# Kernel tuning notes

Hardware: AMD Instinct MI355X
Metric: run time of the kernel (lower is better)

## Reference

```python
import jax, jax.numpy as jnp
import numpy as np

DIM = 768
NUM_HEADS = 12
HEAD_DIM = DIM // NUM_HEADS
SCALE = HEAD_DIM ** -0.5


def setup_inputs() -> dict:
    key = jax.random.key(0)
    k_x, k_qkv, k_pw, k_pb = jax.random.split(key, 4)
    x = jax.random.normal(k_x, (1, 4096, DIM), dtype=jnp.float32)
    # nn.Linear weights stored as [out, in]; apply as x @ W.T
    w_qkv = jax.random.normal(k_qkv, (3 * DIM, DIM), dtype=jnp.float32) * (DIM ** -0.5)
    w_proj = jax.random.normal(k_pw, (DIM, DIM), dtype=jnp.float32) * (DIM ** -0.5)
    b_proj = jax.random.normal(k_pb, (DIM,), dtype=jnp.float32) * 0.01
    return {"x": x, "w_qkv": w_qkv, "w_proj": w_proj, "b_proj": b_proj}


def reference(x, w_qkv, w_proj, b_proj):
    b, s, d = x.shape
    qkv = jnp.einsum('bsd,ed->bse', x, w_qkv)            # [B,S,3D]
    qkv = qkv.reshape(b, s, 3, NUM_HEADS, HEAD_DIM)
    qkv = jnp.transpose(qkv, (2, 0, 3, 1, 4))            # [3,B,H,S,hd]
    q, k, v = qkv[0], qkv[1], qkv[2]
    scores = jnp.einsum('bhqe,bhke->bhqk', q, k) * SCALE  # [B,H,S,S]
    probs = jax.nn.softmax(scores, axis=-1)
    attended = jnp.einsum('bhqk,bhke->bhqe', probs, v)    # [B,H,S,hd]
    attended = jnp.transpose(attended, (0, 2, 1, 3)).reshape(b, s, d)
    return jnp.einsum('bsd,ed->bse', attended, w_proj) + b_proj
```

## Files before the change

### kernel.cpp

```cpp
#include <hip/hip_runtime.h>
#include <hip/hip_bf16.h>

using short8 = __attribute__((ext_vector_type(8))) short;
using s16x4  = __attribute__((ext_vector_type(4))) short;
using f32x2  = __attribute__((ext_vector_type(2))) float;
using f32x4  = __attribute__((ext_vector_type(4))) float;
using f32x16 = __attribute__((ext_vector_type(16))) float;
using v2i    = __attribute__((ext_vector_type(2))) int;

#define DIM   768
#define D3    2304
#define SEQL  4096
#define NHEAD 12
#define NSPLIT 3

#if defined(__has_builtin)
#  if __has_builtin(__builtin_amdgcn_permlane32_swap)
#    define HAVE_PLSWAP 1
#  endif
#endif

static __device__ __forceinline__ short f2bs(float f) {
  union { __hip_bfloat16 h; short s; } u;
  u.h = __float2bfloat16(f);
  return u.s;
}

static __device__ __forceinline__ float bf2f(short s) {
  union { unsigned u; float f; } x;
  x.u = ((unsigned)(unsigned short)s) << 16;
  return x.f;
}

static __device__ __forceinline__ int cvtpk(float lo, float hi) {
  int r;
  asm("v_cvt_pk_bf16_f32 %0, %1, %2" : "=v"(r) : "v"(lo), "v"(hi));
  return r;
}

static __device__ __forceinline__ f32x2 pkadd(f32x2 a, f32x2 b) {
  f32x2 r;
  asm("v_pk_add_f32 %0, %1, %2" : "=v"(r) : "v"(a), "v"(b));
  return r;
}

static __device__ __forceinline__ float ex2(float x) {
  float r;
  asm("v_exp_f32 %0, %1" : "=v"(r) : "v"(x));
  return r;
}

static __device__ __forceinline__ void gl_lds16(const void* g, void* lds) {
  __builtin_amdgcn_global_load_lds((const __attribute__((address_space(1))) void*)g,
                                   (__attribute__((address_space(3))) void*)lds, 16, 0, 0);
}

__global__ __launch_bounds__(256) void cvt3_kernel(const float* __restrict__ x,
                                                   const float* __restrict__ wq,
                                                   const float* __restrict__ wp,
                                                   short* __restrict__ xb,
                                                   short* __restrict__ wqb,
                                                   short* __restrict__ wpb) {
  int b = blockIdx.x;
  const float* src; short* dst; int base; float sc = 1.0f;
  if (b < 3072)      { src = x;  dst = xb;  base = b * 1024; }
  else if (b < 4800) { src = wq; dst = wqb; base = (b - 3072) * 1024;
                       if (base < DIM * DIM) sc = 0.125f * 1.4426950408889634f; }
  else               { src = wp; dst = wpb; base = (b - 4800) * 1024; }
  int i = base + threadIdx.x * 4;
  f32x4 v = *(const f32x4*)(src + i);
  s16x4 o;
  #pragma unroll
  for (int j = 0; j < 4; ++j) o[j] = f2bs(v[j] * sc);
  *(s16x4*)(dst + i) = o;
}

template <bool BF16OUT>
__global__ __launch_bounds__(256) void gemm_bt(const short* __restrict__ A,
                                               const short* __restrict__ B,
                                               short* __restrict__ Cb,
                                               float* __restrict__ Cf,
                                               const float* __restrict__ bias,
                                               int M, int N, int K) {
  __shared__ short As[128 * 64];
  __shared__ short Bs[128 * 64];
  const int tid = threadIdx.x;
  const int l  = tid & 63;
  const int w  = tid >> 6;
  const int g  = l >> 4, lc = l & 15;
  const int wr = w >> 1, wc = w & 1;
  const int m0 = blockIdx.y * 128, n0 = blockIdx.x * 128;
  const int trow = tid >> 3;
  const int tcol = (tid & 7) * 8;

  f32x4 acc[4][4];
  #pragma unroll
  for (int a = 0; a < 4; ++a)
    #pragma unroll
    for (int b = 0; b < 4; ++b) acc[a][b] = (f32x4){0.f, 0.f, 0.f, 0.f};

  for (int k0 = 0; k0 < K; k0 += 64) {
    __syncthreads();
    #pragma unroll
    for (int i = 0; i < 4; ++i) {
      int row = i * 32 + trow;
      gl_lds16(A + (size_t)(m0 + row) * K + k0 + tcol, As + row * 64 + tcol);
      gl_lds16(B + (size_t)(n0 + row) * K + k0 + tcol, Bs + row * 64 + tcol);
    }
    __syncthreads();
    #pragma unroll
    for (int kk = 0; kk < 2; ++kk) {
      short8 af[4], bf[4];
      #pragma unroll
      for (int mt = 0; mt < 4; ++mt)
        af[mt] = *(const short8*)(As + (wr * 64 + mt * 16 + lc) * 64 + kk * 32 + g * 8);
      #pragma unroll
      for (int nt = 0; nt < 4; ++nt)
        bf[nt] = *(const short8*)(Bs + (wc * 64 + nt * 16 + lc) * 64 + kk * 32 + g * 8);
      #pragma unroll
      for (int mt = 0; mt < 4; ++mt)
        #pragma unroll
        for (int nt = 0; nt < 4; ++nt)
          acc[mt][nt] = __builtin_amdgcn_mfma_f32_16x16x32_bf16(af[mt], bf[nt], acc[mt][nt], 0, 0, 0);
    }
  }

  #pragma unroll
  for (int mt = 0; mt < 4; ++mt)
    #pragma unroll
    for (int nt = 0; nt < 4; ++nt)
      #pragma unroll
      for (int r = 0; r < 4; ++r) {
        int row = m0 + wr * 64 + mt * 16 + g * 4 + r;
        int col = n0 + wc * 64 + nt * 16 + lc;
        float v = acc[mt][nt][r];
        if (BF16OUT) Cb[(size_t)row * N + col] = f2bs(v);
        else         Cf[(size_t)row * N + col] = v + bias[col];
      }
}

__global__ __launch_bounds__(256) void transpose_v(const short* __restrict__ qkv,
                                                   short* __restrict__ vtg) {
  __shared__ short T[64][72];
  const int jt = blockIdx.x, hd = blockIdx.y, tid = threadIdx.x;
  #pragma unroll
  for (int i = 0; i < 2; ++i) {
    int idx = i * 256 + tid;
    int r = idx >> 3, c = idx & 7;
    *(short8*)&T[r][8 * c] =
        *(const short8*)(qkv + (size_t)(jt * 64 + r) * D3 + 1536 + hd * 64 + 8 * c);
  }
  __syncthreads();
  #pragma unroll
  for (int i = 0; i < 2; ++i) {
    int idx = i * 256 + tid;
    int d = idx >> 3, jc = idx & 7;
    short8 v;
    #pragma unroll
    for (int e = 0; e < 8; ++e) v[e] = T[8 * jc + e][d];
    *(short8*)(vtg + ((size_t)hd * 64 + d) * 4096 + jt * 64 + 8 * jc) = v;
  }
}

__global__ __launch_bounds__(512) void attn_kernel(const short* __restrict__ qkv,
                                                   const short* __restrict__ vtg,
                                                   short* __restrict__ O0,
                                                   short* __restrict__ O1,
                                                   short* __restrict__ O2,
                                                   float* __restrict__ Lp) {
  __shared__ short Ks[2][64 * 64];
  __shared__ short Vt[2][64 * 64];

  const int tid = threadIdx.x;
  const int l = tid & 63, w = tid >> 6;
  const int h = l >> 5;
  const int q5 = l & 31;
  const int head = blockIdx.y;
  const int hoff = head * 64;
  const int qbase = blockIdx.x * 256 + w * 32;
  const int z = blockIdx.z;
  const int t0 = (z * 64) / 3, tend = ((z + 1) * 64) / 3;

  short8 qf[4];
  {
    const short* qrow = qkv + (size_t)(qbase + q5) * D3 + hoff;
    #pragma unroll
    for (int ks = 0; ks < 4; ++ks) qf[ks] = *(const short8*)(qrow + ks * 16 + h * 8);
  }

  f32x16 o[2];
  #pragma unroll
  for (int nt = 0; nt < 2; ++nt)
    #pragma unroll
    for (int r = 0; r < 16; ++r) o[nt][r] = 0.f;
  float l_run = 0.f;
  const f32x16 zacc = {};

  const int swzK = 8 * (q5 & 7);

  const int srow = tid >> 3, scol = (tid & 7) * 8;
  const int sswz = 8 * (srow & 7);
  const short* kptr = qkv + (size_t)(t0 * 64 + srow) * D3 + hoff + 768 + (scol ^ sswz);
  const short* vptr = vtg + ((size_t)hoff + srow) * 4096 + t0 * 64 + (scol ^ sswz);

  #define STAGE_KV(BUF)                                                          \
    {                                                                            \
      gl_lds16(kptr, &Ks[BUF][tid * 8]);                                         \
      gl_lds16(vptr, &Vt[BUF][tid * 8]);                                         \
      kptr += 64 * D3;                                                           \
      vptr += 64;                                                                \
    }

  STAGE_KV(0);
  asm volatile("s_waitcnt vmcnt(0)" ::: "memory");
  __syncthreads();

  for (int tt = t0; tt < tend; ++tt) {
    const int cur = (tt - t0) & 1;
    const bool pre = (tt + 1 < tend);
    if (pre) STAGE_KV(cur ^ 1);

    f32x16 p[2];
    __builtin_amdgcn_s_setprio(1);
    #pragma unroll
    for (int ks = 0; ks < 4; ++ks) {
      #pragma unroll
      for (int mt = 0; mt < 2; ++mt) {
        short8 kf = *(const short8*)(&Ks[cur][(mt * 32 + q5) * 64
                                              + ((ks * 16 + h * 8) ^ swzK)]);
        p[mt] = __builtin_amdgcn_mfma_f32_32x32x16_bf16(kf, qf[ks],
                                                        ks == 0 ? zacc : p[mt], 0, 0, 0);
      }
    }
    __builtin_amdgcn_s_setprio(0);

    f32x2 s2 = {0.f, 0.f};
    #pragma unroll
    for (int mt = 0; mt < 2; ++mt)
      #pragma unroll
      for (int i = 0; i < 8; ++i) {
        float pe0 = ex2(p[mt][2 * i]);
        float pe1 = ex2(p[mt][2 * i + 1]);
        p[mt][2 * i] = pe0;
        p[mt][2 * i + 1] = pe1;
        s2 = pkadd(s2, (f32x2){pe0, pe1});
      }
    l_run += s2[0] + s2[1];

    int D[16];
    #pragma unroll
    for (int mt = 0; mt < 2; ++mt)
      #pragma unroll
      for (int c = 0; c < 4; ++c) {
        D[mt * 8 + c * 2 + 0] = cvtpk(p[mt][4 * c + 0], p[mt][4 * c + 1]);
        D[mt * 8 + c * 2 + 1] = cvtpk(p[mt][4 * c + 2], p[mt][4 * c + 3]);
      }

    __builtin_amdgcn_s_setprio(1);
    #pragma unroll
    for (int ks = 0; ks < 4; ++ks) {
      union { int i[4]; short8 s; } pa;
#ifdef HAVE_PLSWAP
      v2i r02 = __builtin_amdgcn_permlane32_swap(D[4 * ks + 0], D[4 * ks + 2], false, false);
      v2i r13 = __builtin_amdgcn_permlane32_swap(D[4 * ks + 1], D[4 * ks + 3], false, false);
      pa.i[0] = r02[0];
      pa.i[1] = r13[0];
      pa.i[2] = r02[1];
      pa.i[3] = r13[1];
#else
      const bool hh = (h != 0);
      const int a0 = D[4 * ks + 0], a1 = D[4 * ks + 1];
      const int b0 = D[4 * ks + 2], b1 = D[4 * ks + 3];
      int snd0 = hh ? a0 : b0, snd1 = hh ? a1 : b1;
      int r0 = __shfl_xor(snd0, 32), r1 = __shfl_xor(snd1, 32);
      pa.i[0] = hh ? r0 : a0;
      pa.i[1] = hh ? r1 : a1;
      pa.i[2] = hh ? b0 : r0;
      pa.i[3] = hh ? b1 : r1;
#endif
      #pragma unroll
      for (int nt = 0; nt < 2; ++nt) {
        short8 vf = *(const short8*)(&Vt[cur][(nt * 32 + q5) * 64
                                              + ((ks * 16 + h * 8) ^ swzK)]);
        o[nt] = __builtin_amdgcn_mfma_f32_32x32x16_bf16(pa.s, vf, o[nt], 0, 0, 0);
      }
    }
    __builtin_amdgcn_s_setprio(0);

    asm volatile("s_waitcnt vmcnt(0)" ::: "memory");
    __syncthreads();
  }

  float l_tot = l_run + __shfl_xor(l_run, 32);
  if (h == 0) Lp[(size_t)z * SEQL * NHEAD + (qbase + q5) * NHEAD + head] = l_tot;
  short* Ob = (z == 0) ? O0 : (z == 1) ? O1 : O2;
  #pragma unroll
  for (int nt = 0; nt < 2; ++nt)
    #pragma unroll
    for (int pp = 0; pp < 4; ++pp)
      #pragma unroll
      for (int r = 0; r < 4; ++r) {
        int q = qbase + r + 8 * pp + 4 * h;
        int d = hoff + nt * 32 + q5;
        Ob[(size_t)q * DIM + d] = f2bs(o[nt][4 * pp + r]);
      }
}

__global__ __launch_bounds__(256) void combine_kernel(short* __restrict__ O0,
                                                      const short* __restrict__ O1,
                                                      const short* __restrict__ O2,
                                                      const float* __restrict__ Lp) {
  int idx = blockIdx.x * 256 + threadIdx.x;
  int e0 = idx * 8;
  if (e0 >= SEQL * DIM) return;
  int q = e0 / DIM, col = e0 % DIM, head = col >> 6;
  int i0 = q * NHEAD + head;
  float lv = Lp[i0] + Lp[SEQL * NHEAD + i0] + Lp[2 * SEQL * NHEAD + i0];
  float inv = 1.0f / lv;
  short8 a = *(const short8*)(O0 + e0);
  short8 b = *(const short8*)(O1 + e0);
  short8 c = *(const short8*)(O2 + e0);
  short8 r;
  #pragma unroll
  for (int j = 0; j < 8; ++j)
    r[j] = f2bs((bf2f(a[j]) + bf2f(b[j]) + bf2f(c[j])) * inv);
  *(short8*)(O0 + e0) = r;
}

extern "C" void kernel_launch(void* const* d_in, const int* in_sizes, int n_in,
                              void* d_out, int out_size, void* d_ws, size_t ws_size,
                              hipStream_t stream) {
  (void)in_sizes; (void)n_in; (void)out_size; (void)ws_size;
  const float* x      = (const float*)d_in[0];
  const float* w_qkv  = (const float*)d_in[1];
  const float* w_proj = (const float*)d_in[2];
  const float* b_proj = (const float*)d_in[3];
  float* out = (float*)d_out;

  short* xb   = (short*)d_ws;
  short* wqb  = xb  + (size_t)SEQL * DIM;
  short* wpb  = wqb + (size_t)D3 * DIM;
  short* qkvb = wpb + (size_t)DIM * DIM;
  short* attb = qkvb + (size_t)SEQL * D3;
  short* Opart1 = xb;
  float* Lpart  = (float*)wqb;
  short* vtg    = (short*)d_out;
  short* Opart2 = vtg + (size_t)SEQL * DIM;

  cvt3_kernel<<<5376, 256, 0, stream>>>(x, w_qkv, w_proj, xb, wqb, wpb);
  gemm_bt<true ><<<dim3(D3 / 128, SEQL / 128), 256, 0, stream>>>(xb, wqb, qkvb, nullptr, nullptr, SEQL, D3, DIM);
  transpose_v<<<dim3(SEQL / 64, NHEAD), 256, 0, stream>>>(qkvb, vtg);
  attn_kernel<<<dim3(SEQL / 256, NHEAD, NSPLIT), 512, 0, stream>>>(qkvb, vtg, attb, Opart1, Opart2, Lpart);
  combine_kernel<<<SEQL * DIM / 8 / 256, 256, 0, stream>>>(attb, Opart1, Opart2, Lpart);
  gemm_bt<false><<<dim3(DIM / 128, SEQL / 128), 256, 0, stream>>>(attb, wpb, nullptr, out, b_proj, SEQL, DIM, DIM);
}
```

Before: 156.4 us.

## Triple-buffer KV in attention, shrink blocks, split KV in two, swizzle grid

The attention kernel now uses 256-thread blocks covering 128 queries, with a three-stage K/V ring buffer in LDS. It waits with a partial vmcnt and issues one barrier per tile instead of draining all loads and syncing at the end of each iteration. The KV split drops from three to two, which removes one partial output buffer and simplifies the combine kernel. A linear grid with a swizzled block-to-(query tile, head, split) mapping is meant to improve L2 locality and scheduling. The costs are more LDS per block and less parallelism from the split, offset by more, smaller blocks.

```diff
diff --git a/kernel.cpp b/kernel.cpp
--- a/kernel.cpp
+++ b/kernel.cpp
@@ -12,7 +12,7 @@
 #define D3    2304
 #define SEQL  4096
 #define NHEAD 12
-#define NSPLIT 3
+#define NSPLIT 2
 
 #if defined(__has_builtin)
 #  if __has_builtin(__builtin_amdgcn_permlane32_swap)
@@ -162,24 +162,28 @@
   }
 }
 
-__global__ __launch_bounds__(512) void attn_kernel(const short* __restrict__ qkv,
+__global__ __launch_bounds__(256) void attn_kernel(const short* __restrict__ qkv,
                                                    const short* __restrict__ vtg,
                                                    short* __restrict__ O0,
                                                    short* __restrict__ O1,
-                                                   short* __restrict__ O2,
-                                                   float* __restrict__ Lp) {
-  __shared__ short Ks[2][64 * 64];
-  __shared__ short Vt[2][64 * 64];
+                                                   float* __restrict__ Lp,
+                                                   int tpb) {
+  __shared__ short Ks[3][64 * 64];
+  __shared__ short Vt[3][64 * 64];
+
+  const int lin = blockIdx.x;
+  const int swz = (lin & 7) * 96 + (lin >> 3);
+  const int qt   = swz & 31;
+  const int head = (swz >> 5) % NHEAD;
+  const int z    = swz / (32 * NHEAD);
 
   const int tid = threadIdx.x;
   const int l = tid & 63, w = tid >> 6;
   const int h = l >> 5;
   const int q5 = l & 31;
-  const int head = blockIdx.y;
   const int hoff = head * 64;
-  const int qbase = blockIdx.x * 256 + w * 32;
-  const int z = blockIdx.z;
-  const int t0 = (z * 64) / 3, tend = ((z + 1) * 64) / 3;
+  const int qbase = qt * 128 + w * 32;
+  const int t0 = z * tpb, tend = t0 + tpb;
 
   short8 qf[4];
   {
@@ -203,22 +207,25 @@
   const short* kptr = qkv + (size_t)(t0 * 64 + srow) * D3 + hoff + 768 + (scol ^ sswz);
   const short* vptr = vtg + ((size_t)hoff + srow) * 4096 + t0 * 64 + (scol ^ sswz);
 
-  #define STAGE_KV(BUF)                                                          \
+  #define STAGE(BUF)                                                             \
     {                                                                            \
-      gl_lds16(kptr, &Ks[BUF][tid * 8]);                                         \
-      gl_lds16(vptr, &Vt[BUF][tid * 8]);                                         \
+      gl_lds16(kptr,            &Ks[BUF][tid * 8]);                              \
+      gl_lds16(kptr + 32 * D3,  &Ks[BUF][(tid + 256) * 8]);                      \
+      gl_lds16(vptr,            &Vt[BUF][tid * 8]);                              \
+      gl_lds16(vptr + 32 * 4096, &Vt[BUF][(tid + 256) * 8]);                     \
       kptr += 64 * D3;                                                           \
       vptr += 64;                                                                \
     }
 
-  STAGE_KV(0);
-  asm volatile("s_waitcnt vmcnt(0)" ::: "memory");
-  __syncthreads();
-
+  STAGE(0);
+  STAGE(1);
+
+  int cur = 0, sb = 2;
   for (int tt = t0; tt < tend; ++tt) {
-    const int cur = (tt - t0) & 1;
-    const bool pre = (tt + 1 < tend);
-    if (pre) STAGE_KV(cur ^ 1);
+    if (tt + 1 < tend) asm volatile("s_waitcnt vmcnt(4)" ::: "memory");
+    else               asm volatile("s_waitcnt vmcnt(0)" ::: "memory");
+    __builtin_amdgcn_s_barrier();
+    if (tt + 2 < tend) STAGE(sb);
 
     f32x16 p[2];
     __builtin_amdgcn_s_setprio(1);
@@ -287,13 +294,13 @@
     }
     __builtin_amdgcn_s_setprio(0);
 
-    asm volatile("s_waitcnt vmcnt(0)" ::: "memory");
-    __syncthreads();
+    cur = (cur == 2) ? 0 : cur + 1;
+    sb  = (sb == 2) ? 0 : sb + 1;
   }
 
   float l_tot = l_run + __shfl_xor(l_run, 32);
   if (h == 0) Lp[(size_t)z * SEQL * NHEAD + (qbase + q5) * NHEAD + head] = l_tot;
-  short* Ob = (z == 0) ? O0 : (z == 1) ? O1 : O2;
+  short* Ob = (z == 0) ? O0 : O1;
   #pragma unroll
   for (int nt = 0; nt < 2; ++nt)
     #pragma unroll
@@ -308,22 +315,18 @@
 
 __global__ __launch_bounds__(256) void combine_kernel(short* __restrict__ O0,
                                                       const short* __restrict__ O1,
-                                                      const short* __restrict__ O2,
                                                       const float* __restrict__ Lp) {
   int idx = blockIdx.x * 256 + threadIdx.x;
   int e0 = idx * 8;
   if (e0 >= SEQL * DIM) return;
   int q = e0 / DIM, col = e0 % DIM, head = col >> 6;
-  int i0 = q * NHEAD + head;
-  float lv = Lp[i0] + Lp[SEQL * NHEAD + i0] + Lp[2 * SEQL * NHEAD + i0];
+  float lv = Lp[q * NHEAD + head] + Lp[SEQL * NHEAD + q * NHEAD + head];
   float inv = 1.0f / lv;
   short8 a = *(const short8*)(O0 + e0);
   short8 b = *(const short8*)(O1 + e0);
-  short8 c = *(const short8*)(O2 + e0);
   short8 r;
   #pragma unroll
-  for (int j = 0; j < 8; ++j)
-    r[j] = f2bs((bf2f(a[j]) + bf2f(b[j]) + bf2f(c[j])) * inv);
+  for (int j = 0; j < 8; ++j) r[j] = f2bs((bf2f(a[j]) + bf2f(b[j])) * inv);
   *(short8*)(O0 + e0) = r;
 }
 
@@ -345,12 +348,12 @@
   short* Opart1 = xb;
   float* Lpart  = (float*)wqb;
   short* vtg    = (short*)d_out;
-  short* Opart2 = vtg + (size_t)SEQL * DIM;
 
   cvt3_kernel<<<5376, 256, 0, stream>>>(x, w_qkv, w_proj, xb, wqb, wpb);
   gemm_bt<true ><<<dim3(D3 / 128, SEQL / 128), 256, 0, stream>>>(xb, wqb, qkvb, nullptr, nullptr, SEQL, D3, DIM);
   transpose_v<<<dim3(SEQL / 64, NHEAD), 256, 0, stream>>>(qkvb, vtg);
-  attn_kernel<<<dim3(SEQL / 256, NHEAD, NSPLIT), 512, 0, stream>>>(qkvb, vtg, attb, Opart1, Opart2, Lpart);
-  combine_kernel<<<SEQL * DIM / 8 / 256, 256, 0, stream>>>(attb, Opart1, Opart2, Lpart);
+  attn_kernel<<<dim3(32 * NHEAD * NSPLIT, 1, 1), 256, 0, stream>>>(qkvb, vtg, attb, Opart1, Lpart,
+                                                                   (SEQL / 64) / NSPLIT);
+  combine_kernel<<<SEQL * DIM / 8 / 256, 256, 0, stream>>>(attb, Opart1, Lpart);
   gemm_bt<false><<<dim3(DIM / 128, SEQL / 128), 256, 0, stream>>>(attb, wpb, nullptr, out, b_proj, SEQL, DIM, DIM);
 }
```

After: 147.7 us. 5.6% less time.
